# Kernel tuning notes

Measured on AMD Instinct MI355X. Metric: run time of the kernel, lower is better.

The kernel has to match this reference:

```python
import jax, jax.numpy as jnp
from jax import lax
import numpy as np

B, NQ, NT = 32, 256, 512
INF = jnp.float32(1e30)  # stand-in for float('inf') mask fill; all targets are valid here
W_TRANS, W_QPOS, W_ROT = 1.0, 1.0, 1.0


def setup_inputs() -> dict:
    key = jax.random.key(0)
    k1, k2, k3, k4 = jax.random.split(key, 4)
    rot = jax.random.normal(k3, (B, NQ, 4), jnp.float32)
    rot = rot / jnp.linalg.norm(rot, axis=-1, keepdims=True)  # unit quaternions
    return {
        "translation_norm": jax.random.normal(k1, (B, NQ, 3), jnp.float32),
        "qpos_norm": jax.random.normal(k2, (B, NQ, 16), jnp.float32),
        "rotation": rot,
        "norm_pose": jax.random.normal(k4, (B, NT, 23), jnp.float32),
    }


def _l1_cost(p, t):
    # p: [B, NQ, D], t: [B, NT, D] -> [B, NQ, NT] pairwise L1
    return jnp.abs(p[:, :, None, :] - t[:, None, :, :]).sum(-1)


def _final_cost(translation_norm, qpos_norm, rotation, norm_pose):
    valid = jnp.abs(norm_pose).sum(-1) > 0  # [B, NT]
    cost = (W_TRANS * _l1_cost(translation_norm, norm_pose[..., :3])
            + W_QPOS * _l1_cost(qpos_norm, norm_pose[..., 3:19])
            + W_ROT * (1.0 - jnp.abs(jnp.einsum('bqd,bnd->bqn', rotation, norm_pose[..., 19:]))))
    return jnp.where(valid[:, None, :], cost, INF)


def _hungarian(cost):
    """Rectangular LSAP via Jonker-Volgenant shortest augmenting path
    (same algorithm as scipy.optimize.linear_sum_assignment).
    cost: [n, m] with n <= m. Returns col4row [n]: matched column per row."""
    n, m = cost.shape

    def solve_row(carry, cur_row):
        u, v, col4row, row4col = carry

        # --- Dijkstra-like search for the shortest augmenting path ---
        def s_cond(st):
            return st[6] < 0  # until a free column (sink) is found

        def s_body(st):
            i, minVal, SR, SC, spc, path, _sink = st
            SR = SR.at[i].set(True)
            r = minVal + cost[i] - u[i] - v          # reduced costs for row i
            upd = (~SC) & (r < spc)
            spc = jnp.where(upd, r, spc)
            path = jnp.where(upd, i, path)
            masked = jnp.where(SC, INF, spc)
            j = jnp.argmin(masked).astype(jnp.int32)
            minVal = masked[j]
            SC = SC.at[j].set(True)
            free = row4col[j] < 0
            sink = jnp.where(free, j, jnp.int32(-1))
            i = jnp.where(free, i, row4col[j])
            return (i, minVal, SR, SC, spc, path, sink)

        st0 = (cur_row, jnp.float32(0.0),
               jnp.zeros((n,), bool), jnp.zeros((m,), bool),
               jnp.full((m,), INF), jnp.full((m,), -1, jnp.int32), jnp.int32(-1))
        _i, minVal, SR, SC, spc, path, sink = lax.while_loop(s_cond, s_body, st0)

        # --- dual variable updates ---
        spc_row = spc[jnp.clip(col4row, 0, m - 1)]  # [n]; invalid rows masked by SR
        du = jnp.where(jnp.arange(n) == cur_row, minVal, minVal - spc_row)
        u = u + jnp.where(SR, du, 0.0)
        v = v - jnp.where(SC, minVal - spc, 0.0)

        # --- augment along the alternating path back to cur_row ---
        def a_cond(st):
            return ~st[3]

        def a_body(st):
            j, c4r, r4c, _done = st
            i = path[j]
            r4c = r4c.at[j].set(i)
            nj = c4r[i]
            c4r = c4r.at[i].set(j)
            return (nj, c4r, r4c, i == cur_row)

        _, col4row, row4col, _ = lax.while_loop(
            a_cond, a_body, (sink, col4row, row4col, False))
        return (u, v, col4row, row4col), None

    carry0 = (jnp.zeros((n,), jnp.float32), jnp.zeros((m,), jnp.float32),
              jnp.full((n,), -1, jnp.int32), jnp.full((m,), -1, jnp.int32))
    (u, v, col4row, row4col), _ = lax.scan(
        solve_row, carry0, jnp.arange(n, dtype=jnp.int32))
    return col4row


def reference(translation_norm, qpos_norm, rotation, norm_pose):
    final_cost = _final_cost(translation_norm, qpos_norm, rotation, norm_pose)
    # batched Hungarian (replaces per-batch scipy linear_sum_assignment loop)
    per_query_gt_inds = jax.vmap(_hungarian)(final_cost)        # [B, NQ]
    query_matched_mask = jnp.ones_like(per_query_gt_inds)        # all matched (NT >= NQ)
    return final_cost, per_query_gt_inds, query_matched_mask
```

## Files before the change

### kernel.cpp

```cpp
#include <hip/hip_runtime.h>

constexpr int kB  = 32;
constexpr int kNQ = 256;
constexpr int kNT = 512;
constexpr float kInf = 1e30f;
constexpr int kSlots = 56;
constexpr int kStride = 544;

__device__ __forceinline__ unsigned wave_min_u32(unsigned x) {
    unsigned t;
    t = (unsigned)__builtin_amdgcn_update_dpp((int)0xFFFFFFFF, (int)x, 0x111, 0xF, 0xF, false); x = t < x ? t : x;
    t = (unsigned)__builtin_amdgcn_update_dpp((int)0xFFFFFFFF, (int)x, 0x112, 0xF, 0xF, false); x = t < x ? t : x;
    t = (unsigned)__builtin_amdgcn_update_dpp((int)0xFFFFFFFF, (int)x, 0x114, 0xF, 0xF, false); x = t < x ? t : x;
    t = (unsigned)__builtin_amdgcn_update_dpp((int)0xFFFFFFFF, (int)x, 0x118, 0xF, 0xF, false); x = t < x ? t : x;
    t = (unsigned)__builtin_amdgcn_update_dpp((int)0xFFFFFFFF, (int)x, 0x142, 0xF, 0xF, false); x = t < x ? t : x;
    t = (unsigned)__builtin_amdgcn_update_dpp((int)0xFFFFFFFF, (int)x, 0x143, 0xF, 0xF, false); x = t < x ? t : x;
    return (unsigned)__builtin_amdgcn_readlane((int)x, 63);
}

__global__ __launch_bounds__(512)
void hungarian_kernel(const float* __restrict__ trans,
                      const float* __restrict__ qpos,
                      const float* __restrict__ rot,
                      const float* __restrict__ pose,
                      float* __restrict__ cost,
                      float* __restrict__ outInds,
                      float* __restrict__ outMask)
{
    __shared__ float rowCache[kSlots * kStride];
    __shared__ float u[kNQ];
    __shared__ int   col4row[kNQ];
    __shared__ int   row4col[kNT];
    __shared__ int   colBest[kNT];
    __shared__ int   pathL[kNT];
    __shared__ int   rowArg[kNQ];

    const int b   = blockIdx.x;
    const int tid = threadIdx.x;
    float* __restrict__ Cw = cost + (size_t)b * kNQ * kNT;
    const float* __restrict__ C = Cw;

    float* sPose = rowCache;
    {
        const float* pb = pose + (size_t)b * kNT * 23;
        for (int idx = tid; idx < kNT * 23; idx += 512) sPose[idx] = pb[idx];
    }
    __syncthreads();

    {
        float T[23];
        #pragma unroll
        for (int d = 0; d < 23; ++d) T[d] = sPose[tid * 23 + d];

        float s = 0.f;
        #pragma unroll
        for (int d = 0; d < 23; ++d) s += fabsf(T[d]);
        const bool valid = (s > 0.f);

        const float* tr = trans + (size_t)b * kNQ * 3;
        const float* qp = qpos  + (size_t)b * kNQ * 16;
        const float* rt = rot   + (size_t)b * kNQ * 4;

        for (int q = 0; q < kNQ; ++q) {
            const float Q0 = tr[q * 3 + 0], Q1 = tr[q * 3 + 1], Q2 = tr[q * 3 + 2];
            float a = fabsf(Q0 - T[0]);
            a += fabsf(Q1 - T[1]);
            a += fabsf(Q2 - T[2]);
            float bsum = 0.f;
            #pragma unroll
            for (int d = 0; d < 16; ++d) bsum += fabsf(qp[q * 16 + d] - T[3 + d]);
            const float r0 = rt[q * 4 + 0], r1 = rt[q * 4 + 1];
            const float r2 = rt[q * 4 + 2], r3 = rt[q * 4 + 3];
            float dot = r0 * T[19] + r1 * T[20] + r2 * T[21] + r3 * T[22];
            float c = (a + bsum) + (1.0f - fabsf(dot));
            Cw[(size_t)q * kNT + tid] = valid ? c : kInf;
        }
    }
    __threadfence();
    __syncthreads();

    if (tid < kNQ) {
        const float4* Crow = (const float4*)(C + (size_t)tid * kNT);
        float bm = kInf; int barg = 0;
        #pragma unroll 4
        for (int j4 = 0; j4 < kNT / 4; ++j4) {
            float4 cc = Crow[j4];
            const int jb = j4 * 4;
            if (cc.x < bm) { bm = cc.x; barg = jb + 0; }
            if (cc.y < bm) { bm = cc.y; barg = jb + 1; }
            if (cc.z < bm) { bm = cc.z; barg = jb + 2; }
            if (cc.w < bm) { bm = cc.w; barg = jb + 3; }
        }
        u[tid]      = bm;
        rowArg[tid] = barg;
        col4row[tid] = -1;
    }
    row4col[tid] = -1;
    colBest[tid] = 0x7fffffff;
    __syncthreads();
    if (tid < kNQ) atomicMin(&colBest[rowArg[tid]], tid);
    __syncthreads();
    if (tid < kNQ) {
        const int j = rowArg[tid];
        if (colBest[j] == tid) { col4row[tid] = j; row4col[j] = tid; }
    }
    __syncthreads();

    if (tid < 64) {
        const int lane = tid;
        const int laneOff = (lane >> 3) * 68 + (lane & 7) * 8;
        typedef float v2f __attribute__((ext_vector_type(2)));

        float vR[8];
        #pragma unroll
        for (int c = 0; c < 8; ++c) vR[c] = 0.f;

        int tagReg = -1;
        int rr     = 0;

        for (int cur = 0; cur < kNQ; ++cur) {
            if (col4row[cur] >= 0) continue;

            float spcR[8]; int pathR[8]; float mskA[8]; float frzV[8]; int frzP[8];
            #pragma unroll
            for (int c = 0; c < 8; ++c) {
                spcR[c] = kInf; pathR[c] = -1; mskA[c] = 0.f;
                frzV[c] = 0.f;  frzP[c] = -1;
            }
            unsigned scMask = 0;

            int   i      = cur;
            float minVal = 0.f;
            int   sink   = -1;

            for (int guard = 0; guard < kNT + 2 && sink < 0; ++guard) {
                const float ui = u[i];
                float4 p0, p1;
                const unsigned long long hm = __ballot(tagReg == i);
                if (hm != 0ull) {
                    const int slot = (int)__ffsll(hm) - 1;
                    const float4* lp = (const float4*)&rowCache[slot * kStride + laneOff];
                    p0 = lp[0]; p1 = lp[1];
                } else {
                    const float4* rp = (const float4*)(C + (size_t)i * kNT + lane * 8);
                    p0 = rp[0]; p1 = rp[1];
                    if (guard != 0) {
                        float4* wp = (float4*)&rowCache[rr * kStride + laneOff];
                        wp[0] = p0; wp[1] = p1;
                        if (lane == rr) tagReg = i;
                        rr = rr + 1; if (rr == kSlots) rr = 0;
                    }
                }

                const v2f cc2[4] = { {p0.x, p0.y}, {p0.z, p0.w},
                                     {p1.x, p1.y}, {p1.z, p1.w} };
                const v2f mv2 = { minVal, minVal };
                const v2f ui2 = { ui, ui };
                float r8[8];
                #pragma unroll
                for (int p = 0; p < 4; ++p) {
                    const v2f vv = { vR[2*p], vR[2*p + 1] };
                    const v2f rp2 = ((mv2 + cc2[p]) - ui2) - vv;
                    r8[2*p] = rp2.x; r8[2*p + 1] = rp2.y;
                }
                #pragma unroll
                for (int c = 0; c < 8; ++c) {
                    const bool lt = r8[c] < spcR[c];
                    spcR[c]  = lt ? r8[c] : spcR[c];
                    pathR[c] = lt ? i : pathR[c];
                }

                float mskv[8];
                #pragma unroll
                for (int p = 0; p < 4; ++p) {
                    const v2f s2 = { spcR[2*p], spcR[2*p + 1] };
                    const v2f a2 = { mskA[2*p], mskA[2*p + 1] };
                    const v2f m2 = s2 + a2;
                    mskv[2*p] = m2.x; mskv[2*p + 1] = m2.y;
                }
                unsigned sp[8];
                #pragma unroll
                for (int c = 0; c < 8; ++c) sp[c] = __float_as_uint(mskv[c]);
                unsigned mA = sp[1] < sp[0] ? sp[1] : sp[0]; int aA = sp[1] < sp[0] ? 1 : 0;
                unsigned mB = sp[3] < sp[2] ? sp[3] : sp[2]; int aB = sp[3] < sp[2] ? 3 : 2;
                unsigned mC = sp[5] < sp[4] ? sp[5] : sp[4]; int aC = sp[5] < sp[4] ? 5 : 4;
                unsigned mD = sp[7] < sp[6] ? sp[7] : sp[6]; int aD = sp[7] < sp[6] ? 7 : 6;
                unsigned mAB = mB < mA ? mB : mA; int aAB = mB < mA ? aB : aA;
                unsigned mCD = mD < mC ? mD : mC; int aCD = mD < mC ? aD : aC;
                unsigned lvu = mCD < mAB ? mCD : mAB; int lc = mCD < mAB ? aCD : aAB;
                const int lix  = lane * 8 + lc;
                const int spec = row4col[lix];

                const unsigned gmu = wave_min_u32(lvu);
                const unsigned long long bal = __ballot(lvu == gmu);
                const int wl    = (int)__ffsll(bal) - 1;
                const int jstar = __builtin_amdgcn_readlane(lix, wl);
                const int own   = __builtin_amdgcn_readlane(spec, wl);
                minVal = __uint_as_float(gmu);

                if (own < 0) sink = jstar;
                else         i    = own;

                if (wl == lane) {
                    const int lcw = jstar & 7;
                    scMask |= 1u << lcw;
                    #pragma unroll
                    for (int c = 0; c < 8; ++c) {
                        if (c == lcw) {
                            mskA[c] = __builtin_inff();
                            frzV[c] = minVal;
                            frzP[c] = pathR[c];
                        }
                    }
                }
            }

            if (lane == 0) u[cur] += minVal;
            #pragma unroll
            for (int c = 0; c < 8; ++c) {
                if ((scMask >> c) & 1u) {
                    const int j = lane * 8 + c;
                    const int r = row4col[j];
                    const float d = minVal - frzV[c];
                    if (r >= 0) u[r] += d;
                    vR[c] -= d;
                    pathL[j] = frzP[c];
                }
            }
            __threadfence_block();

            if (lane == 0 && sink >= 0) {
                int j = sink;
                while (true) {
                    const int pi = pathL[j];
                    row4col[j] = pi;
                    const int nj = col4row[pi];
                    col4row[pi] = j;
                    if (pi == cur) break;
                    j = nj;
                }
            }
            __threadfence_block();
        }
    }
    __syncthreads();

    if (tid < kNQ) {
        outInds[(size_t)b * kNQ + tid] = (float)col4row[tid];
        outMask[(size_t)b * kNQ + tid] = 1.0f;
    }
}

extern "C" void kernel_launch(void* const* d_in, const int* in_sizes, int n_in,
                              void* d_out, int out_size, void* d_ws, size_t ws_size,
                              hipStream_t stream) {
    const float* trans = (const float*)d_in[0];
    const float* qpos  = (const float*)d_in[1];
    const float* rot   = (const float*)d_in[2];
    const float* pose  = (const float*)d_in[3];

    float* out  = (float*)d_out;
    float* cost = out;
    float* inds = out + (size_t)kB * kNQ * kNT;
    float* mask = inds + (size_t)kB * kNQ;

    hungarian_kernel<<<kB, 512, 0, stream>>>(trans, qpos, rot, pose, cost, inds, mask);
}
```

Before: 502.1 us.

## Split cost-matrix build across producer blocks with flag-based handoff to solvers

The cost-matrix computation, previously done serially by each of the 32 solver blocks, is moved to 224 extra producer blocks, each computing a 37-query chunk of one batch. Solver blocks spin on a per-batch atomic counter in workspace until all seven chunks are published, then run the Hungarian solve. This spreads the cost build over many CUs, at the price of an extra memset and spin-wait. It relies on producer blocks being scheduled while solvers spin, and a bounded spin count could let solvers proceed on incomplete data.

```diff
diff --git a/kernel.cpp b/kernel.cpp
--- a/kernel.cpp
+++ b/kernel.cpp
@@ -6,6 +6,8 @@
 constexpr float kInf = 1e30f;
 constexpr int kSlots = 56;
 constexpr int kStride = 544;
+constexpr int kChunks = 7;
+constexpr int kQChunk = 37;
 
 __device__ __forceinline__ unsigned wave_min_u32(unsigned x) {
     unsigned t;
@@ -19,13 +21,14 @@
 }
 
 __global__ __launch_bounds__(512)
-void hungarian_kernel(const float* __restrict__ trans,
-                      const float* __restrict__ qpos,
-                      const float* __restrict__ rot,
-                      const float* __restrict__ pose,
-                      float* __restrict__ cost,
-                      float* __restrict__ outInds,
-                      float* __restrict__ outMask)
+void fused_kernel(const float* __restrict__ trans,
+                  const float* __restrict__ qpos,
+                  const float* __restrict__ rot,
+                  const float* __restrict__ pose,
+                  float* __restrict__ cost,
+                  float* __restrict__ outInds,
+                  float* __restrict__ outMask,
+                  unsigned* __restrict__ flags)
 {
     __shared__ float rowCache[kSlots * kStride];
     __shared__ float u[kNQ];
@@ -35,23 +38,23 @@
     __shared__ int   pathL[kNT];
     __shared__ int   rowArg[kNQ];
 
-    const int b   = blockIdx.x;
     const int tid = threadIdx.x;
-    float* __restrict__ Cw = cost + (size_t)b * kNQ * kNT;
-    const float* __restrict__ C = Cw;
-
-    float* sPose = rowCache;
-    {
+
+    if (blockIdx.x >= 32) {
+        const int p     = blockIdx.x - 32;
+        const int b     = p / kChunks;
+        const int chunk = p - b * kChunks;
+        const int q0    = chunk * kQChunk;
+        const int q1    = (q0 + kQChunk < kNQ) ? (q0 + kQChunk) : kNQ;
+
+        float* sPose = rowCache;
         const float* pb = pose + (size_t)b * kNT * 23;
         for (int idx = tid; idx < kNT * 23; idx += 512) sPose[idx] = pb[idx];
-    }
-    __syncthreads();
-
-    {
+        __syncthreads();
+
         float T[23];
         #pragma unroll
         for (int d = 0; d < 23; ++d) T[d] = sPose[tid * 23 + d];
-
         float s = 0.f;
         #pragma unroll
         for (int d = 0; d < 23; ++d) s += fabsf(T[d]);
@@ -60,8 +63,9 @@
         const float* tr = trans + (size_t)b * kNQ * 3;
         const float* qp = qpos  + (size_t)b * kNQ * 16;
         const float* rt = rot   + (size_t)b * kNQ * 4;
-
-        for (int q = 0; q < kNQ; ++q) {
+        float* Cw = cost + (size_t)b * kNQ * kNT;
+
+        for (int q = q0; q < q1; ++q) {
             const float Q0 = tr[q * 3 + 0], Q1 = tr[q * 3 + 1], Q2 = tr[q * 3 + 2];
             float a = fabsf(Q0 - T[0]);
             a += fabsf(Q1 - T[1]);
@@ -75,9 +79,27 @@
             float c = (a + bsum) + (1.0f - fabsf(dot));
             Cw[(size_t)q * kNT + tid] = valid ? c : kInf;
         }
-    }
+
+        __threadfence();
+        __syncthreads();
+        if (tid == 0)
+            __hip_atomic_fetch_add(&flags[b], 1u, __ATOMIC_RELEASE,
+                                   __HIP_MEMORY_SCOPE_AGENT);
+        return;
+    }
+
+    const int b = blockIdx.x;
+    if (tid == 0) {
+        unsigned v = 0; long g = 0;
+        do {
+            v = __hip_atomic_load(&flags[b], __ATOMIC_ACQUIRE,
+                                  __HIP_MEMORY_SCOPE_AGENT);
+        } while (v < (unsigned)kChunks && ++g < (1L << 20));
+    }
+    __syncthreads();
     __threadfence();
-    __syncthreads();
+
+    const float* __restrict__ C = cost + (size_t)b * kNQ * kNT;
 
     if (tid < kNQ) {
         const float4* Crow = (const float4*)(C + (size_t)tid * kNT);
@@ -264,5 +286,8 @@
     float* inds = out + (size_t)kB * kNQ * kNT;
     float* mask = inds + (size_t)kB * kNQ;
 
-    hungarian_kernel<<<kB, 512, 0, stream>>>(trans, qpos, rot, pose, cost, inds, mask);
+    unsigned* flags = (unsigned*)d_ws;
+    hipMemsetAsync(d_ws, 0, kB * sizeof(unsigned), stream);
+    fused_kernel<<<dim3(32 + kB * kChunks), 512, 0, stream>>>(
+        trans, qpos, rot, pose, cost, inds, mask, flags);
 }
```

After: 489.8 us. -2.4%, faster.
